# Performance work log

Hardware: AMD Instinct MI355X
Metric: run time of the kernel (lower is better)

Reference implementation:

```python
import jax, jax.numpy as jnp
from jax import lax
import numpy as np


def _qlayer(x, theta):
    """Simulate QLayer: RX(x_i) encoder + trainable RX(theta_i) per wire
    (they commute -> single RX(x_i+theta_i) on |0>), then ring of CNOTs,
    then <Z> on each wire.  x: (B, n) float, theta: (n,). Returns (B, n)."""
    B, n = x.shape
    a = x + theta[None, :]
    c = jnp.cos(a * 0.5)
    s = jnp.sin(a * 0.5)
    # RX(a)|0> = [cos(a/2), -i sin(a/2)] per wire -> product state
    amps = jnp.stack([c + 0j, -1j * s], axis=-1)  # (B, n, 2) complex64
    state = amps[:, 0]  # (B, 2)
    for w in range(1, n):
        state = state[..., None] * amps[:, w].reshape((B,) + (1,) * w + (2,))
    # state: (B, 2, 2, ..., 2), axis w+1 == wire w
    for ctrl in range(n):
        tgt = (ctrl + 1) % n
        s0 = jnp.take(state, 0, axis=ctrl + 1)   # control = 0 block
        s1 = jnp.take(state, 1, axis=ctrl + 1)   # control = 1 block
        t_ax = tgt + 1 if tgt < ctrl else tgt    # target axis after removing ctrl axis
        s1 = jnp.flip(s1, axis=t_ax)             # X on target
        state = jnp.stack([s0, s1], axis=ctrl + 1)
    p = state.real ** 2 + state.imag ** 2
    axes = tuple(range(1, n + 1))
    zs = []
    for w in range(n):
        other = tuple(ax for ax in axes if ax != w + 1)
        pw = jnp.sum(p, axis=other)              # (B, 2)
        zs.append(pw[:, 0] - pw[:, 1])           # <Z_w> = P(0) - P(1)
    return jnp.stack(zs, axis=1)


def setup_inputs() -> dict:
    key = jax.random.key(0)
    ks = jax.random.split(key, 13)
    T, B, D, NQ = 64, 256, 512, 6
    lim = 1.0 / np.sqrt(D + NQ)

    def lin(k):
        k1, k2 = jax.random.split(k)
        W = jax.random.uniform(k1, (D + NQ, NQ), jnp.float32, -lim, lim)
        b = jax.random.uniform(k2, (NQ,), jnp.float32, -lim, lim)
        return W, b

    Wf, bf = lin(ks[0]); Wi, bi = lin(ks[1]); Wu, bu = lin(ks[2]); Wo, bo = lin(ks[3])
    theta_f = jax.random.normal(ks[4], (NQ,), jnp.float32) * 0.1
    theta_i = jax.random.normal(ks[5], (NQ,), jnp.float32) * 0.1
    theta_u = jax.random.normal(ks[6], (NQ,), jnp.float32) * 0.1
    theta_o = jax.random.normal(ks[7], (NQ,), jnp.float32) * 0.1
    inputs = jax.random.normal(ks[8], (T, B, D), jnp.float32)
    return {"inputs": inputs,
            "Wf": Wf, "bf": bf, "Wi": Wi, "bi": bi,
            "Wu": Wu, "bu": bu, "Wo": Wo, "bo": bo,
            "theta_f": theta_f, "theta_i": theta_i,
            "theta_u": theta_u, "theta_o": theta_o}


def reference(inputs, Wf, bf, Wi, bi, Wu, bu, Wo, bo,
              theta_f, theta_i, theta_u, theta_o):
    B = inputs.shape[1]
    NQ = theta_f.shape[0]  # hidden_dim == n_qubits
    h0 = jnp.zeros((B, NQ), inputs.dtype)
    c0 = jnp.zeros((B, NQ), inputs.dtype)

    def step(carry, x):
        hx, cx = carry
        comb = jnp.concatenate([x, hx], axis=1)          # (B, D+NQ)
        f = jax.nn.sigmoid(_qlayer(comb @ Wf + bf, theta_f))
        i = jax.nn.sigmoid(_qlayer(comb @ Wi + bi, theta_i))
        g = jnp.tanh(_qlayer(comb @ Wu + bu, theta_u))
        o = jax.nn.sigmoid(_qlayer(comb @ Wo + bo, theta_o))
        cx2 = f * cx + i * g
        hx2 = o * jnp.tanh(cx2)
        return (hx2, cx2), hx2

    (hx, cx), outputs = lax.scan(step, (h0, c0), inputs)  # outputs: (T, B, NQ)
    return outputs, hx, cx
```

## Files before the change

kernel.cpp:

```cpp
#include <hip/hip_runtime.h>


__device__ __forceinline__ float fast_rcp(float x) { return __builtin_amdgcn_rcpf(x); }

template <int G>
__device__ __forceinline__ float quad_bcast(float v) {
    int i = __builtin_amdgcn_ds_swizzle(__float_as_int(v), 0x8000 | (G * 0x55));
    return __int_as_float(i);
}

__global__ __launch_bounds__(256) void gemm_pre(
    const float* __restrict__ X,
    const float* __restrict__ Wf, const float* __restrict__ bf,
    const float* __restrict__ Wi, const float* __restrict__ bi,
    const float* __restrict__ Wu, const float* __restrict__ bu,
    const float* __restrict__ Wo, const float* __restrict__ bo,
    const float* __restrict__ thf, const float* __restrict__ thi,
    const float* __restrict__ thu, const float* __restrict__ tho,
    float* __restrict__ pre)
{
    __shared__ float Buf[6144];
    __shared__ float Bs[24];

    const int tid = threadIdx.x;
    if (tid < 24) {
        int g = tid / 6, w = tid % 6;
        const float* bb = (g==0)?bf:(g==1)?bi:(g==2)?bu:bo;
        const float* tt = (g==0)?thf:(g==1)?thi:(g==2)?thu:tho;
        Bs[tid] = bb[w] + tt[w];
    }

    const int r    = tid & 63;
    const int ksub = tid >> 6;
    const int kuni = __builtin_amdgcn_readfirstlane(ksub << 4);
    const int rowbase = blockIdx.x * 64;

    const int srow = tid >> 4;
    const int sk4  = tid & 15;

    float acc[24];
    #pragma unroll
    for (int j = 0; j < 24; ++j) acc[j] = 0.f;

    float4 pf[4];
    #pragma unroll
    for (int i = 0; i < 4; ++i)
        pf[i] = *(const float4*)(X + (rowbase + srow + i*16)*512 + 0 + sk4*4);

    for (int kb = 0; kb < 512; kb += 64) {
        __syncthreads();
        #pragma unroll
        for (int i = 0; i < 4; ++i)
            *(float4*)(&Buf[(srow + i*16)*68 + sk4*4]) = pf[i];
        __syncthreads();
        if (kb < 448) {
            #pragma unroll
            for (int i = 0; i < 4; ++i)
                pf[i] = *(const float4*)(X + (rowbase + srow + i*16)*512 + (kb + 64) + sk4*4);
        }
        #pragma unroll
        for (int kk4 = 0; kk4 < 4; ++kk4) {
            float4 a4 = *(const float4*)(&Buf[r*68 + kuni + kk4*4]);
            float av[4] = {a4.x, a4.y, a4.z, a4.w};
            #pragma unroll
            for (int q = 0; q < 4; ++q) {
                const int k = kb + kuni + kk4*4 + q;
                const float a = av[q];
                #pragma unroll
                for (int gg = 0; gg < 4; ++gg) {
                    const float* Wp = (gg==0)?Wf:(gg==1)?Wi:(gg==2)?Wu:Wo;
                    const float2* pw = (const float2*)(Wp + k*6);
                    float2 w0 = pw[0], w1 = pw[1], w2 = pw[2];
                    acc[gg*6+0] = fmaf(a, w0.x, acc[gg*6+0]);
                    acc[gg*6+1] = fmaf(a, w0.y, acc[gg*6+1]);
                    acc[gg*6+2] = fmaf(a, w1.x, acc[gg*6+2]);
                    acc[gg*6+3] = fmaf(a, w1.y, acc[gg*6+3]);
                    acc[gg*6+4] = fmaf(a, w2.x, acc[gg*6+4]);
                    acc[gg*6+5] = fmaf(a, w2.y, acc[gg*6+5]);
                }
            }
        }
    }

    __syncthreads();
    {
        float4* dst = (float4*)&Buf[(ksub*64 + r)*24];
        dst[0] = make_float4(acc[0],  acc[1],  acc[2],  acc[3]);
        dst[1] = make_float4(acc[4],  acc[5],  acc[6],  acc[7]);
        dst[2] = make_float4(acc[8],  acc[9],  acc[10], acc[11]);
        dst[3] = make_float4(acc[12], acc[13], acc[14], acc[15]);
        dst[4] = make_float4(acc[16], acc[17], acc[18], acc[19]);
        dst[5] = make_float4(acc[20], acc[21], acc[22], acc[23]);
    }
    __syncthreads();
    #pragma unroll
    for (int i = 0; i < 6; ++i) {
        int f  = i*256 + tid;
        int rr = f / 24, j = f % 24;
        float s = Buf[rr*24 + j] + Buf[1536 + rr*24 + j]
                + Buf[3072 + rr*24 + j] + Buf[4608 + rr*24 + j] + Bs[j];
        pre[(rowbase + rr)*24 + j] = s;
    }
}

__global__ __launch_bounds__(64, 1) void qlstm_scan(
    const float* __restrict__ pre,
    const float* __restrict__ Wf, const float* __restrict__ Wi,
    const float* __restrict__ Wu, const float* __restrict__ Wo,
    float* __restrict__ out)
{
    const int lane = threadIdx.x;
    const int bl   = lane >> 2;
    const int g    = lane & 3;
    const int b    = blockIdx.x * 16 + bl;

    const float* Wg = (g==0)?Wf:(g==1)?Wi:(g==2)?Wu:Wo;
    float Wh[6][6];
    #pragma unroll
    for (int j = 0; j < 6; ++j)
        #pragma unroll
        for (int w = 0; w < 6; ++w)
            Wh[j][w] = Wg[(512 + j)*6 + w];

    const float k1 = (g==2) ? 2.f : 1.f;
    const float k2 = (g==2) ? 2.f : 1.f;
    const float k3 = (g==2) ? -1.f : 0.f;

    float h[6], c[6];
    #pragma unroll
    for (int w = 0; w < 6; ++w) { h[w] = 0.f; c[w] = 0.f; }

    const float* p0 = pre + b*24 + g*6;
    float2 x0 = *(const float2*)(p0);
    float2 x1 = *(const float2*)(p0 + 2);
    float2 x2 = *(const float2*)(p0 + 4);

    for (int t = 0; t < 64; ++t) {
        float xw[6] = {x0.x, x0.y, x1.x, x1.y, x2.x, x2.y};
        int tn = (t < 63) ? (t + 1) : 63;
        const float* pn = pre + (tn*256 + b)*24 + g*6;
        x0 = *(const float2*)(pn);
        x1 = *(const float2*)(pn + 2);
        x2 = *(const float2*)(pn + 4);

        float a[6];
        #pragma unroll
        for (int w = 0; w < 6; ++w) a[w] = xw[w];
        #pragma unroll
        for (int j = 0; j < 6; ++j)
            #pragma unroll
            for (int w = 0; w < 6; ++w)
                a[w] = fmaf(h[j], Wh[j][w], a[w]);

        float C[6];
        #pragma unroll
        for (int w = 0; w < 6; ++w) C[w] = __cosf(a[w]);

        float p01 = C[0]*C[1], p23 = C[2]*C[3], p45 = C[4]*C[5];
        float z[6];
        z[1] = p01;
        z[2] = p01*C[2];
        z[3] = p01*p23;
        z[4] = z[3]*C[4];
        z[5] = z[3]*p45;
        z[0] = C[1]*(p23*p45);

        float act[6];
        #pragma unroll
        for (int w = 0; w < 6; ++w) {
            float e = __expf(-k1 * z[w]);
            act[w] = fmaf(k2, fast_rcp(1.f + e), k3);
        }

        float F[6], I[6], U[6], O[6];
        #pragma unroll
        for (int w = 0; w < 6; ++w) {
            F[w] = quad_bcast<0>(act[w]);
            I[w] = quad_bcast<1>(act[w]);
            U[w] = quad_bcast<2>(act[w]);
            O[w] = quad_bcast<3>(act[w]);
        }

        #pragma unroll
        for (int w = 0; w < 6; ++w) {
            c[w] = fmaf(F[w], c[w], I[w]*U[w]);
            float e  = __expf(-2.f * c[w]);
            float tc = fmaf(2.f, fast_rcp(1.f + e), -1.f);
            h[w] = O[w]*tc;
        }

        if (g < 3) {
            float2 v;
            v.x = (g==0) ? h[0] : (g==1) ? h[2] : h[4];
            v.y = (g==0) ? h[1] : (g==1) ? h[3] : h[5];
            *(float2*)(out + (t*256 + b)*6 + g*2) = v;
        }
    }

    if (g < 3) {
        float2 v;
        v.x = (g==0) ? h[0] : (g==1) ? h[2] : h[4];
        v.y = (g==0) ? h[1] : (g==1) ? h[3] : h[5];
        *(float2*)(out + 64*256*6 + b*6 + g*2) = v;
        float2 u;
        u.x = (g==0) ? c[0] : (g==1) ? c[2] : c[4];
        u.y = (g==0) ? c[1] : (g==1) ? c[3] : c[5];
        *(float2*)(out + 64*256*6 + 256*6 + b*6 + g*2) = u;
    }
}

extern "C" void kernel_launch(void* const* d_in, const int* in_sizes, int n_in,
                              void* d_out, int out_size, void* d_ws, size_t ws_size,
                              hipStream_t stream) {
    const float* X   = (const float*)d_in[0];
    const float* Wf  = (const float*)d_in[1];
    const float* bf_ = (const float*)d_in[2];
    const float* Wi  = (const float*)d_in[3];
    const float* bi_ = (const float*)d_in[4];
    const float* Wu  = (const float*)d_in[5];
    const float* bu_ = (const float*)d_in[6];
    const float* Wo  = (const float*)d_in[7];
    const float* bo_ = (const float*)d_in[8];
    const float* thf = (const float*)d_in[9];
    const float* thi = (const float*)d_in[10];
    const float* thu = (const float*)d_in[11];
    const float* tho = (const float*)d_in[12];

    float* pre = (float*)d_ws;
    float* out = (float*)d_out;

    gemm_pre<<<256, 256, 0, stream>>>(X, Wf, bf_, Wi, bi_, Wu, bu_, Wo, bo_,
                                      thf, thi, thu, tho, pre);
    qlstm_scan<<<16, 64, 0, stream>>>(pre, Wf, Wi, Wu, Wo, out);
}
```

Before: 160.1 us.

## Restructure input projection GEMM with LDS-staged weights and DPP reductions

The input-projection kernel now stages all four gate weight matrices (512x24) in LDS once per block. Each lane owns one k column and computes 4 rows with packed v2f FMAs, reading X directly from global memory with coalesced lane-contiguous loads instead of tiling X through LDS. Partial sums are reduced across lanes with DPP adds and then through LDS, and the launch doubles to 512 blocks of 512 threads. The quad broadcast in the scan kernel also switches from ds_swizzle to DPP. The aim is to stop re-reading weights from global or cache in the inner loop, at the cost of a large per-block LDS weight load and a multi-stage reduction.

```diff
diff --git a/kernel.cpp b/kernel.cpp
--- a/kernel.cpp
+++ b/kernel.cpp
@@ -1,15 +1,23 @@
 #include <hip/hip_runtime.h>
 
 
+typedef float v2f __attribute__((ext_vector_type(2)));
+
 __device__ __forceinline__ float fast_rcp(float x) { return __builtin_amdgcn_rcpf(x); }
+
+template <int CTRL>
+__device__ __forceinline__ float dpp_add(float x) {
+    int t = __builtin_amdgcn_mov_dpp(__float_as_int(x), CTRL, 0xF, 0xF, true);
+    return x + __int_as_float(t);
+}
 
 template <int G>
 __device__ __forceinline__ float quad_bcast(float v) {
-    int i = __builtin_amdgcn_ds_swizzle(__float_as_int(v), 0x8000 | (G * 0x55));
+    int i = __builtin_amdgcn_mov_dpp(__float_as_int(v), G * 0x55, 0xF, 0xF, true);
     return __int_as_float(i);
 }
 
-__global__ __launch_bounds__(256) void gemm_pre(
+__global__ __launch_bounds__(512, 3) void gemm_pre(
     const float* __restrict__ X,
     const float* __restrict__ Wf, const float* __restrict__ bf,
     const float* __restrict__ Wi, const float* __restrict__ bi,
@@ -19,87 +27,82 @@
     const float* __restrict__ thu, const float* __restrict__ tho,
     float* __restrict__ pre)
 {
-    __shared__ float Buf[6144];
-    __shared__ float Bs[24];
-
-    const int tid = threadIdx.x;
-    if (tid < 24) {
-        int g = tid / 6, w = tid % 6;
+    __shared__ float W_lds[13312];
+
+    const int tid  = threadIdx.x;
+    const int w    = tid >> 6;
+    const int lane = tid & 63;
+    const int rowbase = blockIdx.x * 32;
+
+    #pragma unroll
+    for (int i = 0; i < 4; ++i) {
+        const float* Wp = (i==0)?Wf:(i==1)?Wi:(i==2)?Wu:Wo;
+        int k = tid;
+        const float2* s = (const float2*)(Wp + k*6);
+        float2* d = (float2*)(W_lds + k*26 + i*6);
+        d[0] = s[0]; d[1] = s[1]; d[2] = s[2];
+    }
+    __syncthreads();
+
+    v2f acc[4][12];
+    #pragma unroll
+    for (int r = 0; r < 4; ++r)
+        #pragma unroll
+        for (int p = 0; p < 12; ++p) acc[r][p] = (v2f){0.f, 0.f};
+
+    const float* Xr0 = X + (rowbase + w*4)*512 + lane;
+
+    #pragma unroll
+    for (int kb = 0; kb < 512; kb += 64) {
+        float a0 = Xr0[kb];
+        float a1 = Xr0[kb + 512];
+        float a2 = Xr0[kb + 1024];
+        float a3 = Xr0[kb + 1536];
+        const v2f* wrow = (const v2f*)(W_lds + (kb + lane)*26);
+        #pragma unroll
+        for (int p = 0; p < 12; ++p) {
+            v2f wv = wrow[p];
+            acc[0][p] = __builtin_elementwise_fma((v2f){a0,a0}, wv, acc[0][p]);
+            acc[1][p] = __builtin_elementwise_fma((v2f){a1,a1}, wv, acc[1][p]);
+            acc[2][p] = __builtin_elementwise_fma((v2f){a2,a2}, wv, acc[2][p]);
+            acc[3][p] = __builtin_elementwise_fma((v2f){a3,a3}, wv, acc[3][p]);
+        }
+    }
+
+    float* af = (float*)acc;
+    #pragma unroll
+    for (int v = 0; v < 96; ++v) {
+        float x = af[v];
+        x = dpp_add<0xB1>(x);
+        x = dpp_add<0x4E>(x);
+        af[v] = x;
+    }
+
+    __syncthreads();
+    {
+        const int q = lane >> 2;
+        const int j = lane & 3;
+        #pragma unroll
+        for (int i = 0; i < 24; ++i) {
+            int v = i*4 + j;
+            W_lds[(w*96 + v)*16 + q] = af[v];
+        }
+    }
+    __syncthreads();
+
+    for (int o = tid; o < 768; o += 512) {
+        int ww = o / 96, v = o - ww*96;
+        int rr = v / 24, j = v - rr*24;
+        const float4* rp = (const float4*)(W_lds + (ww*96 + v)*16);
+        float4 r0 = rp[0], r1 = rp[1], r2 = rp[2], r3 = rp[3];
+        float s = ((r0.x+r0.y)+(r0.z+r0.w)) + ((r1.x+r1.y)+(r1.z+r1.w))
+                + ((r2.x+r2.y)+(r2.z+r2.w)) + ((r3.x+r3.y)+(r3.z+r3.w));
+        int g = j / 6, jj = j - g*6;
         const float* bb = (g==0)?bf:(g==1)?bi:(g==2)?bu:bo;
         const float* tt = (g==0)?thf:(g==1)?thi:(g==2)?thu:tho;
-        Bs[tid] = bb[w] + tt[w];
-    }
-
-    const int r    = tid & 63;
-    const int ksub = tid >> 6;
-    const int kuni = __builtin_amdgcn_readfirstlane(ksub << 4);
-    const int rowbase = blockIdx.x * 64;
-
-    const int srow = tid >> 4;
-    const int sk4  = tid & 15;
-
-    float acc[24];
-    #pragma unroll
-    for (int j = 0; j < 24; ++j) acc[j] = 0.f;
-
-    float4 pf[4];
-    #pragma unroll
-    for (int i = 0; i < 4; ++i)
-        pf[i] = *(const float4*)(X + (rowbase + srow + i*16)*512 + 0 + sk4*4);
-
-    for (int kb = 0; kb < 512; kb += 64) {
-        __syncthreads();
-        #pragma unroll
-        for (int i = 0; i < 4; ++i)
-            *(float4*)(&Buf[(srow + i*16)*68 + sk4*4]) = pf[i];
-        __syncthreads();
-        if (kb < 448) {
-            #pragma unroll
-            for (int i = 0; i < 4; ++i)
-                pf[i] = *(const float4*)(X + (rowbase + srow + i*16)*512 + (kb + 64) + sk4*4);
-        }
-        #pragma unroll
-        for (int kk4 = 0; kk4 < 4; ++kk4) {
-            float4 a4 = *(const float4*)(&Buf[r*68 + kuni + kk4*4]);
-            float av[4] = {a4.x, a4.y, a4.z, a4.w};
-            #pragma unroll
-            for (int q = 0; q < 4; ++q) {
-                const int k = kb + kuni + kk4*4 + q;
-                const float a = av[q];
-                #pragma unroll
-                for (int gg = 0; gg < 4; ++gg) {
-                    const float* Wp = (gg==0)?Wf:(gg==1)?Wi:(gg==2)?Wu:Wo;
-                    const float2* pw = (const float2*)(Wp + k*6);
-                    float2 w0 = pw[0], w1 = pw[1], w2 = pw[2];
-                    acc[gg*6+0] = fmaf(a, w0.x, acc[gg*6+0]);
-                    acc[gg*6+1] = fmaf(a, w0.y, acc[gg*6+1]);
-                    acc[gg*6+2] = fmaf(a, w1.x, acc[gg*6+2]);
-                    acc[gg*6+3] = fmaf(a, w1.y, acc[gg*6+3]);
-                    acc[gg*6+4] = fmaf(a, w2.x, acc[gg*6+4]);
-                    acc[gg*6+5] = fmaf(a, w2.y, acc[gg*6+5]);
-                }
-            }
-        }
-    }
-
-    __syncthreads();
-    {
-        float4* dst = (float4*)&Buf[(ksub*64 + r)*24];
-        dst[0] = make_float4(acc[0],  acc[1],  acc[2],  acc[3]);
-        dst[1] = make_float4(acc[4],  acc[5],  acc[6],  acc[7]);
-        dst[2] = make_float4(acc[8],  acc[9],  acc[10], acc[11]);
-        dst[3] = make_float4(acc[12], acc[13], acc[14], acc[15]);
-        dst[4] = make_float4(acc[16], acc[17], acc[18], acc[19]);
-        dst[5] = make_float4(acc[20], acc[21], acc[22], acc[23]);
-    }
-    __syncthreads();
-    #pragma unroll
-    for (int i = 0; i < 6; ++i) {
-        int f  = i*256 + tid;
-        int rr = f / 24, j = f % 24;
-        float s = Buf[rr*24 + j] + Buf[1536 + rr*24 + j]
-                + Buf[3072 + rr*24 + j] + Buf[4608 + rr*24 + j] + Bs[j];
-        pre[(rowbase + rr)*24 + j] = s;
+        s += bb[jj] + tt[jj];
+        int row = rowbase + ww*4 + rr;
+        pre[row*24 + j] = s;
     }
 }
 
@@ -229,7 +232,7 @@
     float* pre = (float*)d_ws;
     float* out = (float*)d_out;
 
-    gemm_pre<<<256, 256, 0, stream>>>(X, Wf, bf_, Wi, bi_, Wu, bu_, Wo, bo_,
+    gemm_pre<<<512, 512, 0, stream>>>(X, Wf, bf_, Wi, bi_, Wu, bu_, Wo, bo_,
                                       thf, thi, thu, tho, pre);
     qlstm_scan<<<16, 64, 0, stream>>>(pre, Wf, Wi, Wu, Wo, out);
 }
```

Result: slower. 313.6 us (+95.9%).
